# Kernel optimization log

Hardware: AMD Instinct MI355X
Metric: run time of the kernel (lower is better)

The kernel has to match this reference:

```python
import jax, jax.numpy as jnp
import numpy as np

B, T, Tc = 64, 256, 16
VW, VC, L = 100000, 128, 25
CE, CH = 25, 25          # char embed / char lstm hidden per direction
WE, WH = 100, 100        # word embed / word lstm hidden per direction (bi -> 200)
DW = WE + 2 * CH         # 150, word-LSTM input dim


def lstm(x, Wih, Whh, b):
    """Unidirectional LSTM over time axis 1. x: [N, S, D] -> [N, S, H]. PyTorch gate order i,f,g,o."""
    N = x.shape[0]
    H = Whh.shape[0]
    x_t = jnp.swapaxes(x, 0, 1)  # [S, N, D]

    def step(carry, xt):
        h, c = carry
        g = xt @ Wih + h @ Whh + b
        i, f, gg, o = jnp.split(g, 4, axis=-1)
        c = jax.nn.sigmoid(f) * c + jax.nn.sigmoid(i) * jnp.tanh(gg)
        h = jax.nn.sigmoid(o) * jnp.tanh(c)
        return (h, c), h

    h0 = jnp.zeros((N, H), x.dtype)
    _, hs = jax.lax.scan(step, (h0, h0), x_t)
    return jnp.swapaxes(hs, 0, 1)  # [N, S, H]


def crf_nll(em, tags, trans, start, end):
    """Negative log-likelihood of linear-chain CRF (no mask; full-length sequences)."""
    # gold path score
    em_score = jnp.take_along_axis(em, tags[:, :, None], axis=2).squeeze(-1).sum(axis=1)
    tr_score = trans[tags[:, :-1], tags[:, 1:]].sum(axis=1)
    gold = start[tags[:, 0]] + em_score + tr_score + end[tags[:, -1]]
    # forward algorithm (log partition)
    alpha0 = start[None, :] + em[:, 0]  # [B, L]

    def step(alpha, e_t):
        # alpha: [B, L] prev-tag scores; trans: [L, L]; e_t: [B, L]
        new = jax.nn.logsumexp(alpha[:, :, None] + trans[None, :, :] + e_t[:, None, :], axis=1)
        return new, None

    alpha, _ = jax.lax.scan(step, alpha0, jnp.swapaxes(em[:, 1:], 0, 1))
    logZ = jax.nn.logsumexp(alpha + end[None, :], axis=1)
    return jnp.sum(logZ - gold)


def setup_inputs():
    key = jax.random.key(0)
    ks = jax.random.split(key, 24)
    f = lambda i, shape: jax.random.normal(ks[i], shape, jnp.float32) * 0.1
    return {
        "tok_tensor": jax.random.randint(ks[0], (B, T), 0, VW),
        "tag_tensor": jax.random.randint(ks[1], (B, T), 0, L),
        "lengths": jnp.full((B,), T, jnp.int32),
        "char_tensor": jax.random.randint(ks[2], (B * T, Tc), 0, VC),
        "char_lengths": jax.random.randint(ks[3], (B * T,), 1, Tc + 1),
        "char_tensor_recover": jax.random.permutation(ks[4], B * T),
        "word_emb": f(5, (VW, WE)),
        "char_emb": f(6, (VC, CE)),
        "cWih_f": f(7, (CE, 4 * CH)), "cWhh_f": f(8, (CH, 4 * CH)), "cb_f": jnp.zeros((4 * CH,), jnp.float32),
        "cWih_b": f(9, (CE, 4 * CH)), "cWhh_b": f(10, (CH, 4 * CH)), "cb_b": jnp.zeros((4 * CH,), jnp.float32),
        "wWih_f": f(11, (DW, 4 * WH)), "wWhh_f": f(12, (WH, 4 * WH)), "wb_f": jnp.zeros((4 * WH,), jnp.float32),
        "wWih_b": f(13, (DW, 4 * WH)), "wWhh_b": f(14, (WH, 4 * WH)), "wb_b": jnp.zeros((4 * WH,), jnp.float32),
        "W_tag": f(15, (2 * WH, L)), "b_tag": jnp.zeros((L,), jnp.float32),
        "trans": f(16, (L, L)), "start": f(17, (L,)), "end": f(18, (L,)),
    }


def reference(tok_tensor, tag_tensor, lengths, char_tensor, char_lengths, char_tensor_recover,
              word_emb, char_emb,
              cWih_f, cWhh_f, cb_f, cWih_b, cWhh_b, cb_b,
              wWih_f, wWhh_f, wb_f, wWih_b, wWhh_b, wb_b,
              W_tag, b_tag, trans, start, end):
    N = char_tensor.shape[0]  # B*T words
    # ---- char BiLSTM: last hidden of each direction per word ----
    ce = char_emb[char_tensor]                      # [N, Tc, CE]
    last = char_lengths - 1
    hf = lstm(ce, cWih_f, cWhh_f, cb_f)             # [N, Tc, CH]
    h_fwd = hf[jnp.arange(N), last]                 # forward last valid hidden
    # backward: reverse each word within its length, scan, take hidden at step len-1
    t_ar = jnp.arange(Tc)[None, :]
    rev_idx = jnp.where(t_ar < char_lengths[:, None], char_lengths[:, None] - 1 - t_ar, t_ar)
    ce_rev = jnp.take_along_axis(ce, rev_idx[:, :, None], axis=1)
    hb = lstm(ce_rev, cWih_b, cWhh_b, cb_b)
    h_bwd = hb[jnp.arange(N), last]
    char_feat = jnp.concatenate([h_fwd, h_bwd], axis=-1)[char_tensor_recover].reshape(B, T, 2 * CH)
    # ---- concat word + char features (dropout = identity in eval) ----
    x = jnp.concatenate([word_emb[tok_tensor], char_feat], axis=-1)  # [B, T, DW]
    # ---- word BiLSTM (full-length sequences) ----
    h_f = lstm(x, wWih_f, wWhh_f, wb_f)
    h_b = jnp.flip(lstm(jnp.flip(x, axis=1), wWih_b, wWhh_b, wb_b), axis=1)
    seq = jnp.concatenate([h_f, h_b], axis=-1)       # [B, T, 2*WH]
    # ---- emissions + CRF NLL ----
    em = seq @ W_tag + b_tag                         # [B, T, L]
    return crf_nll(em, tag_tensor, trans, start, end)
```

## Files before the change

kernel.cpp:

```cpp
#include <hip/hip_runtime.h>
#include <hip/hip_bf16.h>

#define NB 64
#define NT 256
#define TC 16
#define NL 25
#define NWORDS 16384
#define DWd 150
#define WEd 100
#define WPB 5

__device__ __forceinline__ float sigf(float x){ return __fdividef(1.f, 1.f + __expf(-x)); }
__device__ __forceinline__ float tanhf_(float x){
    float ax = fabsf(x);
    float e = __expf(-2.f*ax);
    float r = (1.f - e) * __fdividef(1.f, 1.f + e);
    return copysignf(r, x);
}
__device__ __forceinline__ float RL(float v, int k){
    return __int_as_float(__builtin_amdgcn_readlane(__float_as_int(v), k));
}

__global__ void k_gxc(const float* __restrict__ char_emb,
                      const float* __restrict__ cWih_f, const float* __restrict__ cb_f,
                      const float* __restrict__ cWih_b, const float* __restrict__ cb_b,
                      float* __restrict__ gxc){
  int i = blockIdx.x*blockDim.x + threadIdx.x;
  if (i >= 128*2*100) return;
  int col = i % 100; int d = (i/100) & 1; int c = i/200;
  const float* Wih = d ? cWih_b : cWih_f;
  const float* bb  = d ? cb_b  : cb_f;
  float acc = bb[col];
  #pragma unroll
  for (int k=0;k<25;k++) acc += char_emb[c*25+k]*Wih[k*100+col];
  gxc[i] = acc;
}

__global__ __launch_bounds__(512) void k_char(const int* __restrict__ char_tensor,
   const int* __restrict__ char_lengths,
   const float* __restrict__ cWhh_f, const float* __restrict__ cWhh_b,
   const float* __restrict__ gxc, float* __restrict__ cf){
  __shared__ float h_lds[WPB][28];
  __shared__ float act[WPB][100];
  __shared__ int   chars[WPB][TC];
  __shared__ int   lens[WPB];
  int tid = threadIdx.x;
  int d  = blockIdx.x & 1;
  int wb = blockIdx.x >> 1;
  int w0 = wb*WPB;
  if (tid < WPB*TC){
    int ww = w0 + tid/TC;
    int cw = ww < NWORDS ? ww : NWORDS-1;
    chars[tid/TC][tid%TC] = char_tensor[cw*TC + (tid%TC)];
  }
  if (tid < WPB){
    int ww = w0 + tid;
    lens[tid] = char_lengths[ww < NWORDS ? ww : NWORDS-1];
  }
  int wsub = tid/100;
  int j    = tid - wsub*100;
  bool gate_thr = tid < WPB*100;
  const float* Wh = d ? cWhh_b : cWhh_f;
  float wcol[25];
  if (gate_thr){
    #pragma unroll
    for (int k=0;k<25;k++) wcol[k] = Wh[k*100 + j];
  }
  if (gate_thr && j < 28) h_lds[wsub][j] = 0.f;
  float c_reg = 0.f, h_last = 0.f;
  __syncthreads();
  int len = gate_thr ? lens[wsub] : 1;
  bool isg = (j >= 50) && (j < 75);
  float gnext = 0.f;
  if (gate_thr){
    int ci = d ? (len-1) : 0;
    if (ci < 0 || ci >= TC) ci = 0;
    gnext = gxc[(size_t)(chars[wsub][ci]*2+d)*100 + j];
  }
  for (int t=0;t<TC;t++){
    float gcur = gnext;
    if (gate_thr && t+1 < TC){
      int ci = d ? (len-2-t) : (t+1);
      if (ci < 0 || ci >= TC) ci = 0;
      gnext = gxc[(size_t)(chars[wsub][ci]*2+d)*100 + j];
    }
    if (gate_thr){
      float a = gcur;
      const float4* h4 = (const float4*)h_lds[wsub];
      #pragma unroll
      for (int kq=0;kq<6;kq++){
        float4 hq = h4[kq];
        a += hq.x*wcol[4*kq] + hq.y*wcol[4*kq+1] + hq.z*wcol[4*kq+2] + hq.w*wcol[4*kq+3];
      }
      a += h_lds[wsub][24]*wcol[24];
      act[wsub][j] = isg ? tanhf_(a) : sigf(a);
    }
    __syncthreads();
    if (gate_thr && j < 25 && t < len){
      float si = act[wsub][j], sf = act[wsub][25+j], sg = act[wsub][50+j], so = act[wsub][75+j];
      c_reg = sf*c_reg + si*sg;
      float hv = so*tanhf_(c_reg);
      h_lds[wsub][j] = hv;
      h_last = hv;
    }
    __syncthreads();
  }
  if (gate_thr && j < 25){
    int w = w0 + wsub;
    if (w < NWORDS) cf[(size_t)w*56 + d*28 + j] = h_last;
  }
}

__global__ __launch_bounds__(256) void k_wih(const int* __restrict__ tok,
    const int* __restrict__ recover,
    const float* __restrict__ word_emb, const float* __restrict__ cf,
    const float* __restrict__ Wf, const float* __restrict__ bf,
    const float* __restrict__ Wb, const float* __restrict__ bbias,
    float* __restrict__ gx){
  __shared__ float As[150][72];
  __shared__ int toks[64], recs[64];
  int tid = threadIdx.x;
  int m0 = (blockIdx.x>>2)*64;
  int nt = blockIdx.x & 3;
  int n0 = nt*256;
  if (tid < 64) toks[tid] = tok[m0 + tid];
  else if (tid < 128) recs[tid-64] = recover[m0 + tid - 64];
  __syncthreads();
  for (int i=tid; i<64*150; i+=256){
    int r = i/150; int k = i - r*150;
    float v;
    if (k < WEd) v = word_emb[(long)toks[r]*WEd + k];
    else {
      int ci = k - WEd;
      int dd = ci/25; int uu = ci - dd*25;
      v = cf[(size_t)recs[r]*56 + dd*28 + uu];
    }
    As[k][r] = v;
  }
  __syncthreads();
  int tn = tid & 31; int tm = tid >> 5;
  int j0 = n0 + tn*8;
  bool colok = j0 < 800;
  int d = (j0 >= 400) ? 1 : 0;
  const float* W = d ? Wb : Wf;
  int jc = j0 - d*400;
  float acc[8][8];
  #pragma unroll
  for (int mi=0;mi<8;mi++)
    #pragma unroll
    for (int ni=0;ni<8;ni++) acc[mi][ni]=0.f;
  if (colok){
    for (int k=0;k<150;k++){
      float4 b0 = *(const float4*)&W[k*400 + jc];
      float4 b1 = *(const float4*)&W[k*400 + jc + 4];
      float4 a0 = *(const float4*)&As[k][tm*8];
      float4 a1 = *(const float4*)&As[k][tm*8+4];
      float av[8] = {a0.x,a0.y,a0.z,a0.w,a1.x,a1.y,a1.z,a1.w};
      float bv[8] = {b0.x,b0.y,b0.z,b0.w,b1.x,b1.y,b1.z,b1.w};
      #pragma unroll
      for (int mi=0;mi<8;mi++)
        #pragma unroll
        for (int ni=0;ni<8;ni++) acc[mi][ni] += av[mi]*bv[ni];
    }
    const float* bptr = d ? bbias : bf;
    float bias[8];
    #pragma unroll
    for (int ni=0;ni<8;ni++) bias[ni] = bptr[jc+ni];
    #pragma unroll
    for (int mi=0;mi<8;mi++){
      int p = m0 + tm*8 + mi;
      float* orow = gx + ((long)d*NWORDS + p)*400 + jc;
      #pragma unroll
      for (int ni=0;ni<8;ni++) orow[ni] = acc[mi][ni] + bias[ni];
    }
  }
}

__global__ __launch_bounds__(448, 2) void k_wlstm(const float* __restrict__ gx,
     const float* __restrict__ Whf, const float* __restrict__ Whb,
     float* __restrict__ hseq){
  __shared__ float wstage[10000];
  __shared__ float h_lds[100];
  __shared__ float act[400];
  int tid = threadIdx.x;
  int s = blockIdx.x & 63; int d = blockIdx.x >> 6;
  const float* Wh = d ? Whb : Whf;
  int j = tid;
  bool colthr = j < 400;
  float wreg[100];
  #pragma unroll
  for (int ch=0; ch<4; ch++){
    for (int i=tid; i<2500; i+=448)
      ((float4*)wstage)[i] = ((const float4*)(Wh + ch*10000))[i];
    __syncthreads();
    if (colthr){
      #pragma unroll
      for (int kk=0;kk<25;kk++) wreg[ch*25+kk] = wstage[kk*400 + j];
    }
    __syncthreads();
  }
  if (tid < 100) h_lds[tid] = 0.f;
  float c_reg = 0.f;
  const float* gxd = gx + ((long)d*NWORDS + (long)s*256)*400;
  bool isg = (j >= 200) && (j < 300);
  __syncthreads();
  float gnext = 0.f;
  if (colthr) gnext = gxd[(d?255:0)*400 + j];
  for (int t=0;t<256;t++){
    float gcur = gnext;
    if (colthr && t+1 < 256){
      int tn = d ? (255-(t+1)) : (t+1);
      gnext = gxd[tn*400 + j];
    }
    if (colthr){
      float a = gcur;
      const float4* h4 = (const float4*)h_lds;
      #pragma unroll
      for (int kq=0;kq<25;kq++){
        float4 hq = h4[kq];
        a += hq.x*wreg[4*kq] + hq.y*wreg[4*kq+1] + hq.z*wreg[4*kq+2] + hq.w*wreg[4*kq+3];
      }
      act[j] = isg ? tanhf_(a) : sigf(a);
    }
    __syncthreads();
    if (tid < 100){
      float si = act[tid], sf = act[100+tid], sg = act[200+tid], so = act[300+tid];
      c_reg = sf*c_reg + si*sg;
      float hv = so*tanhf_(c_reg);
      h_lds[tid] = hv;
      int ttc = d ? (255-t) : t;
      hseq[((long)d*NWORDS + s*256 + ttc)*100 + tid] = hv;
    }
    __syncthreads();
  }
}

__global__ __launch_bounds__(256) void k_em(const float* __restrict__ hseq,
    const float* __restrict__ Wtag, const float* __restrict__ btag,
    float* __restrict__ em){
  __shared__ float hrow[8][200];
  __shared__ float Ws[5000];
  int tid = threadIdx.x;
  for (int i=tid;i<5000;i+=256) Ws[i] = Wtag[i];
  int p0 = blockIdx.x*8;
  for (int i=tid;i<8*200;i+=256){
    int r = i/200; int k = i - r*200;
    int p = p0+r;
    hrow[r][k] = (k<100) ? hseq[(long)p*100+k] : hseq[((long)NWORDS + p)*100 + (k-100)];
  }
  __syncthreads();
  int r = tid>>5; int c = tid&31;
  if (c<25){
    float acc = btag[c];
    for (int k=0;k<200;k++) acc += hrow[r][k]*Ws[k*25+c];
    em[(long)(p0+r)*25 + c] = acc;
  }
}

__global__ __launch_bounds__(64) void k_crf(const float* __restrict__ em,
    const int* __restrict__ tag, const float* __restrict__ trans,
    const float* __restrict__ start, const float* __restrict__ endv,
    float* __restrict__ part){
  int s = blockIdx.x;
  int lane = threadIdx.x;
  const float* emb = em + (long)s*256*25;
  float tr[25];
  #pragma unroll
  for (int k=0;k<25;k++) tr[k] = (lane<25) ? trans[k*25+lane] : 0.f;
  float alpha = (lane<25) ? (start[lane] + emb[lane]) : 0.f;
  float enext = (lane<25) ? emb[25+lane] : 0.f;
  for (int t=1;t<256;t++){
    float ecur = enext;
    if (t<255 && lane<25) enext = emb[(t+1)*25 + lane];
    float base = RL(alpha, 0);
    float s0=0.f,s1=0.f,s2=0.f,s3=0.f,s4=0.f;
    #pragma unroll
    for (int k=0;k<5;k++) s0 += __expf(RL(alpha,k)    + tr[k]    - base);
    #pragma unroll
    for (int k=0;k<5;k++) s1 += __expf(RL(alpha,5+k)  + tr[5+k]  - base);
    #pragma unroll
    for (int k=0;k<5;k++) s2 += __expf(RL(alpha,10+k) + tr[10+k] - base);
    #pragma unroll
    for (int k=0;k<5;k++) s3 += __expf(RL(alpha,15+k) + tr[15+k] - base);
    #pragma unroll
    for (int k=0;k<5;k++) s4 += __expf(RL(alpha,20+k) + tr[20+k] - base);
    float ssum = ((s0+s1)+(s2+s3))+s4;
    alpha = __logf(ssum) + base + ecur;
  }
  float val = (lane<25) ? (alpha + endv[lane]) : -1e30f;
  float m2 = -1e30f;
  #pragma unroll
  for (int k=0;k<25;k++) m2 = fmaxf(m2, RL(val,k));
  float s2s = 0.f;
  #pragma unroll
  for (int k=0;k<25;k++) s2s += __expf(RL(val,k) - m2);
  float logZ = __logf(s2s) + m2;
  const int* tg = tag + s*256;
  float gp = 0.f;
  for (int t=lane; t<256; t+=64){
    int a = tg[t];
    gp += emb[t*25 + a];
    if (t<255) gp += trans[a*25 + tg[t+1]];
  }
  #pragma unroll
  for (int off=32; off; off>>=1) gp += __shfl_xor(gp, off, 64);
  if (lane==0){
    float gold = gp + start[tg[0]] + endv[tg[255]];
    part[s] = logZ - gold;
  }
}

__global__ __launch_bounds__(64) void k_red(const float* __restrict__ part, float* __restrict__ out){
  float v = part[threadIdx.x];
  #pragma unroll
  for (int off=32; off; off>>=1) v += __shfl_xor(v, off, 64);
  if (threadIdx.x==0) out[0] = v;
}

extern "C" void kernel_launch(void* const* d_in, const int* in_sizes, int n_in,
                              void* d_out, int out_size, void* d_ws, size_t ws_size,
                              hipStream_t stream){
  const int* tok          = (const int*)d_in[0];
  const int* tagp         = (const int*)d_in[1];
  const int* char_tensor  = (const int*)d_in[3];
  const int* char_lengths = (const int*)d_in[4];
  const int* recover      = (const int*)d_in[5];
  const float* word_emb = (const float*)d_in[6];
  const float* char_emb = (const float*)d_in[7];
  const float* cWih_f=(const float*)d_in[8];  const float* cWhh_f=(const float*)d_in[9];  const float* cb_f=(const float*)d_in[10];
  const float* cWih_b=(const float*)d_in[11]; const float* cWhh_b=(const float*)d_in[12]; const float* cb_b=(const float*)d_in[13];
  const float* wWih_f=(const float*)d_in[14]; const float* wWhh_f=(const float*)d_in[15]; const float* wb_f=(const float*)d_in[16];
  const float* wWih_b=(const float*)d_in[17]; const float* wWhh_b=(const float*)d_in[18]; const float* wb_b=(const float*)d_in[19];
  const float* W_tag=(const float*)d_in[20];  const float* b_tag=(const float*)d_in[21];
  const float* trans=(const float*)d_in[22];  const float* startv=(const float*)d_in[23]; const float* endv=(const float*)d_in[24];

  float* ws  = (float*)d_ws;
  float* gxc = ws;
  float* cf  = ws + 25600;
  float* gx  = ws + 943104;
  float* hseq= ws + 14050304;
  float* em  = ws;
  float* part= ws + 17327104;
  float* out = (float*)d_out;

  k_gxc   <<<100, 256, 0, stream>>>(char_emb, cWih_f, cb_f, cWih_b, cb_b, gxc);
  k_char  <<<6554,512, 0, stream>>>(char_tensor, char_lengths, cWhh_f, cWhh_b, gxc, cf);
  k_wih   <<<1024,256, 0, stream>>>(tok, recover, word_emb, cf, wWih_f, wb_f, wWih_b, wb_b, gx);
  k_wlstm <<<128, 448, 0, stream>>>(gx, wWhh_f, wWhh_b, hseq);
  k_em    <<<2048,256, 0, stream>>>(hseq, W_tag, b_tag, em);
  k_crf   <<<64,  64,  0, stream>>>(em, tagp, trans, startv, endv, part);
  k_red   <<<1,   64,  0, stream>>>(part, out);
}
```

Measured before the change: 566.2 us.

## Bucket words by char length so char LSTM blocks stop at max length

Adds histogram, scan and scatter kernels that sort word indices by character length. The char LSTM kernel then reads its words through this index and loops only up to the longest word in its block, not always 16 steps. This cuts padded recurrence steps and their barriers when lengths vary. In exchange it adds four small launches and indirect gathers of chars and outputs.

```diff
diff --git a/kernel.cpp b/kernel.cpp
--- a/kernel.cpp
+++ b/kernel.cpp
@@ -19,6 +19,42 @@
 }
 __device__ __forceinline__ float RL(float v, int k){
     return __int_as_float(__builtin_amdgcn_readlane(__float_as_int(v), k));
+}
+
+__global__ void k_zero(int* __restrict__ meta){
+  if (threadIdx.x < 34) meta[threadIdx.x] = 0;
+}
+__global__ __launch_bounds__(256) void k_hist(const int* __restrict__ char_lengths,
+                                              int* __restrict__ hist){
+  __shared__ int lh[16];
+  int tid = threadIdx.x;
+  if (tid < 16) lh[tid] = 0;
+  __syncthreads();
+  int w = blockIdx.x*256 + tid;
+  atomicAdd(&lh[char_lengths[w]-1], 1);
+  __syncthreads();
+  if (tid < 16) atomicAdd(&hist[tid], lh[tid]);
+}
+__global__ void k_scan(const int* __restrict__ hist, int* __restrict__ cursor){
+  if (threadIdx.x == 0){
+    int acc = 0;
+    for (int i=0;i<16;i++){ cursor[i] = acc; acc += hist[i]; }
+  }
+}
+__global__ __launch_bounds__(256) void k_scatter(const int* __restrict__ char_lengths,
+                                                 int* __restrict__ cursor,
+                                                 int* __restrict__ widx){
+  __shared__ int lh[16], lbase[16];
+  int tid = threadIdx.x;
+  if (tid < 16) lh[tid] = 0;
+  __syncthreads();
+  int w = blockIdx.x*256 + tid;
+  int len = char_lengths[w]-1;
+  int lrank = atomicAdd(&lh[len], 1);
+  __syncthreads();
+  if (tid < 16) lbase[tid] = atomicAdd(&cursor[tid], lh[tid]);
+  __syncthreads();
+  widx[lbase[len] + lrank] = w;
 }
 
 __global__ void k_gxc(const float* __restrict__ char_emb,
@@ -37,26 +73,28 @@
 }
 
 __global__ __launch_bounds__(512) void k_char(const int* __restrict__ char_tensor,
-   const int* __restrict__ char_lengths,
+   const int* __restrict__ char_lengths, const int* __restrict__ widx,
    const float* __restrict__ cWhh_f, const float* __restrict__ cWhh_b,
    const float* __restrict__ gxc, float* __restrict__ cf){
   __shared__ float h_lds[WPB][28];
   __shared__ float act[WPB][100];
   __shared__ int   chars[WPB][TC];
   __shared__ int   lens[WPB];
+  __shared__ int   wids[WPB];
   int tid = threadIdx.x;
   int d  = blockIdx.x & 1;
   int wb = blockIdx.x >> 1;
   int w0 = wb*WPB;
+  if (tid < WPB){
+    int slot = w0 + tid; if (slot > NWORDS-1) slot = NWORDS-1;
+    wids[tid] = widx[slot];
+  }
+  __syncthreads();
   if (tid < WPB*TC){
-    int ww = w0 + tid/TC;
-    int cw = ww < NWORDS ? ww : NWORDS-1;
-    chars[tid/TC][tid%TC] = char_tensor[cw*TC + (tid%TC)];
-  }
-  if (tid < WPB){
-    int ww = w0 + tid;
-    lens[tid] = char_lengths[ww < NWORDS ? ww : NWORDS-1];
-  }
+    int ww = wids[tid/TC];
+    chars[tid/TC][tid%TC] = char_tensor[ww*TC + (tid%TC)];
+  }
+  if (tid < WPB) lens[tid] = char_lengths[wids[tid]];
   int wsub = tid/100;
   int j    = tid - wsub*100;
   bool gate_thr = tid < WPB*100;
@@ -69,6 +107,9 @@
   if (gate_thr && j < 28) h_lds[wsub][j] = 0.f;
   float c_reg = 0.f, h_last = 0.f;
   __syncthreads();
+  int lmax = lens[0];
+  #pragma unroll
+  for (int q=1;q<WPB;q++) lmax = max(lmax, lens[q]);
   int len = gate_thr ? lens[wsub] : 1;
   bool isg = (j >= 50) && (j < 75);
   float gnext = 0.f;
@@ -77,7 +118,7 @@
     if (ci < 0 || ci >= TC) ci = 0;
     gnext = gxc[(size_t)(chars[wsub][ci]*2+d)*100 + j];
   }
-  for (int t=0;t<TC;t++){
+  for (int t=0;t<lmax;t++){
     float gcur = gnext;
     if (gate_thr && t+1 < TC){
       int ci = d ? (len-2-t) : (t+1);
@@ -106,8 +147,8 @@
     __syncthreads();
   }
   if (gate_thr && j < 25){
-    int w = w0 + wsub;
-    if (w < NWORDS) cf[(size_t)w*56 + d*28 + j] = h_last;
+    int w = wids[wsub];
+    cf[(size_t)w*56 + d*28 + j] = h_last;
   }
 }
 
@@ -341,13 +382,19 @@
   float* hseq= ws + 14050304;
   float* em  = ws;
   float* part= ws + 17327104;
+  int*   meta= (int*)(ws + 17327168);
+  int*   widx= meta + 64;
   float* out = (float*)d_out;
 
-  k_gxc   <<<100, 256, 0, stream>>>(char_emb, cWih_f, cb_f, cWih_b, cb_b, gxc);
-  k_char  <<<6554,512, 0, stream>>>(char_tensor, char_lengths, cWhh_f, cWhh_b, gxc, cf);
-  k_wih   <<<1024,256, 0, stream>>>(tok, recover, word_emb, cf, wWih_f, wb_f, wWih_b, wb_b, gx);
-  k_wlstm <<<128, 448, 0, stream>>>(gx, wWhh_f, wWhh_b, hseq);
-  k_em    <<<2048,256, 0, stream>>>(hseq, W_tag, b_tag, em);
-  k_crf   <<<64,  64,  0, stream>>>(em, tagp, trans, startv, endv, part);
-  k_red   <<<1,   64,  0, stream>>>(part, out);
-}
+  k_zero   <<<1,   64,  0, stream>>>(meta);
+  k_gxc    <<<100, 256, 0, stream>>>(char_emb, cWih_f, cb_f, cWih_b, cb_b, gxc);
+  k_hist   <<<64,  256, 0, stream>>>(char_lengths, meta);
+  k_scan   <<<1,   64,  0, stream>>>(meta, meta+16);
+  k_scatter<<<64,  256, 0, stream>>>(char_lengths, meta+16, widx);
+  k_char   <<<6554,512, 0, stream>>>(char_tensor, char_lengths, widx, cWhh_f, cWhh_b, gxc, cf);
+  k_wih    <<<1024,256, 0, stream>>>(tok, recover, word_emb, cf, wWih_f, wb_f, wWih_b, wb_b, gx);
+  k_wlstm  <<<128, 448, 0, stream>>>(gx, wWhh_f, wWhh_b, hseq);
+  k_em     <<<2048,256, 0, stream>>>(hseq, W_tag, b_tag, em);
+  k_crf    <<<64,  64,  0, stream>>>(em, tagp, trans, startv, endv, part);
+  k_red    <<<1,   64,  0, stream>>>(part, out);
+}
```

After: 540.3 us. -4.6%, faster.
